# Optimization experiments

Measured on AMD Instinct MI355X. Metric: run time of the kernel, lower is better.

Reference implementation:

```python
import jax, jax.numpy as jnp
import numpy as np

B, S, D, H, DK, F, L, V = 4, 128, 512, 8, 64, 2048, 2, 32000
N = B * S  # nodes per side (enc and dec each)


def _pe():
    pos = np.arange(S, dtype=np.float32)[:, None]
    div = np.exp(-np.log(10000.0) * np.arange(0, D, 2, dtype=np.float32) / D)
    pe = np.zeros((S, D), dtype=np.float32)
    pe[:, 0::2] = np.sin(pos * div)
    pe[:, 1::2] = np.cos(pos * div)
    return jnp.asarray(np.tile(pe, (B, 1)))  # [N, D]


def _ln(x, g, b, eps=1e-5):
    mu = jnp.mean(x, -1, keepdims=True)
    var = jnp.mean(jnp.square(x - mu), -1, keepdims=True)
    return g * (x - mu) * jax.lax.rsqrt(var + eps) + b


def _edge_attn(q, k, v, src, dst, n_dst):
    # src_dot_dst('k','q','score') then scaled_exp, then src_mul_edge + sum scatter
    s = jnp.sum(k[src] * q[dst], -1, keepdims=True) / np.float32(np.sqrt(DK))  # [E,H,1]
    s = jnp.exp(jnp.clip(s, -10.0, 10.0))
    wv = jax.ops.segment_sum(v[src] * s, dst, num_segments=n_dst)  # [n_dst,H,DK]
    z = jax.ops.segment_sum(s, dst, num_segments=n_dst)            # [n_dst,H,1]
    return wv / z


def _attn_block(x_q, x_kv, Wq, Wk, Wv, Wo, src, dst):
    q = (x_q @ Wq).reshape(-1, H, DK)
    k = (x_kv @ Wk).reshape(-1, H, DK)
    v = (x_kv @ Wv).reshape(-1, H, DK)
    o = _edge_attn(q, k, v, src, dst, x_q.shape[0]).reshape(-1, D)
    return o @ Wo


def _forward(p, src_tok, tgt_tok, ee_src, ee_dst, dd_src, dd_dst, ed_src, ed_dst):
    (src_emb, tgt_emb, enc_Wqkv, enc_Wo, enc_ln1, enc_W1, enc_b1, enc_W2, enc_b2,
     enc_ln2, enc_lnf, dec_Wqkv, dec_Wo, dec_ln1, dec_cWq, dec_cWkv, dec_cWo,
     dec_ln2, dec_W1, dec_b1, dec_W2, dec_b2, dec_ln3, dec_lnf, gen_W, gen_b) = p
    pe = _pe()
    scale = np.float32(np.sqrt(D))
    x_e = src_emb[src_tok].reshape(N, D) * scale + pe  # token + positional embed
    x_d = tgt_emb[tgt_tok].reshape(N, D) * scale + pe
    for l in range(L):  # encoder layers (ee edges)
        xn = _ln(x_e, enc_ln1[l, 0], enc_ln1[l, 1])
        x_e = x_e + _attn_block(xn, xn, enc_Wqkv[l, 0], enc_Wqkv[l, 1], enc_Wqkv[l, 2], enc_Wo[l], ee_src, ee_dst)
        xn = _ln(x_e, enc_ln2[l, 0], enc_ln2[l, 1])
        x_e = x_e + jax.nn.relu(xn @ enc_W1[l] + enc_b1[l]) @ enc_W2[l] + enc_b2[l]
    x_e = _ln(x_e, enc_lnf[0], enc_lnf[1])
    for l in range(L):  # decoder layers: self (dd) then cross (ed)
        xn = _ln(x_d, dec_ln1[l, 0], dec_ln1[l, 1])
        x_d = x_d + _attn_block(xn, xn, dec_Wqkv[l, 0], dec_Wqkv[l, 1], dec_Wqkv[l, 2], dec_Wo[l], dd_src, dd_dst)
        xn = _ln(x_d, dec_ln2[l, 0], dec_ln2[l, 1])
        x_d = x_d + _attn_block(xn, x_e, dec_cWq[l], dec_cWkv[l, 0], dec_cWkv[l, 1], dec_cWo[l], ed_src, ed_dst)
        xn = _ln(x_d, dec_ln3[l, 0], dec_ln3[l, 1])
        x_d = x_d + jax.nn.relu(xn @ dec_W1[l] + dec_b1[l]) @ dec_W2[l] + dec_b2[l]
    x_d = _ln(x_d, dec_lnf[0], dec_lnf[1])
    return jax.nn.log_softmax(x_d @ gen_W + gen_b, axis=-1)  # generator


def setup_inputs():
    key = jax.random.key(0)
    ks = iter(jax.random.split(key, 32))
    w = lambda *shape: jax.random.normal(next(ks), shape, jnp.float32) * 0.02
    lnp = lambda n: jnp.tile(jnp.stack([jnp.ones(D), jnp.zeros(D)])[None], (n, 1, 1))
    # structured edge lists: per-sentence blocks
    i, j = np.meshgrid(np.arange(S), np.arange(S), indexing='ij')  # src pos, dst pos
    base = (np.arange(B)[:, None] * S).astype(np.int32)
    full_s = (base + i.ravel()[None, :]).ravel().astype(np.int32)
    full_d = (base + j.ravel()[None, :]).ravel().astype(np.int32)
    m = i.ravel() <= j.ravel()  # causal mask for dec self-attention
    dd_s = (base + i.ravel()[m][None, :]).ravel().astype(np.int32)
    dd_d = (base + j.ravel()[m][None, :]).ravel().astype(np.int32)
    k1, k2 = jax.random.split(next(ks))
    return dict(
        src_emb=w(V, D), tgt_emb=w(V, D),
        enc_Wqkv=w(L, 3, D, D), enc_Wo=w(L, D, D), enc_ln1=lnp(L),
        enc_W1=w(L, D, F), enc_b1=jnp.zeros((L, F)), enc_W2=w(L, F, D),
        enc_b2=jnp.zeros((L, D)), enc_ln2=lnp(L), enc_lnf=lnp(1)[0],
        dec_Wqkv=w(L, 3, D, D), dec_Wo=w(L, D, D), dec_ln1=lnp(L),
        dec_cWq=w(L, D, D), dec_cWkv=w(L, 2, D, D), dec_cWo=w(L, D, D), dec_ln2=lnp(L),
        dec_W1=w(L, D, F), dec_b1=jnp.zeros((L, F)), dec_W2=w(L, F, D),
        dec_b2=jnp.zeros((L, D)), dec_ln3=lnp(L), dec_lnf=lnp(1)[0],
        gen_W=w(D, V), gen_b=jnp.zeros((V,)),
        src_tok=jax.random.randint(k1, (B, S), 0, V, jnp.int32),
        tgt_tok=jax.random.randint(k2, (B, S), 0, V, jnp.int32),
        ee_src=jnp.asarray(full_s), ee_dst=jnp.asarray(full_d),
        dd_src=jnp.asarray(dd_s), dd_dst=jnp.asarray(dd_d),
        ed_src=jnp.asarray(full_s), ed_dst=jnp.asarray(full_d),
    )


def reference(src_emb, tgt_emb, enc_Wqkv, enc_Wo, enc_ln1, enc_W1, enc_b1, enc_W2,
              enc_b2, enc_ln2, enc_lnf, dec_Wqkv, dec_Wo, dec_ln1, dec_cWq,
              dec_cWkv, dec_cWo, dec_ln2, dec_W1, dec_b1, dec_W2, dec_b2,
              dec_ln3, dec_lnf, gen_W, gen_b, src_tok, tgt_tok, ee_src, ee_dst,
              dd_src, dd_dst, ed_src, ed_dst):
    p = (src_emb, tgt_emb, enc_Wqkv, enc_Wo, enc_ln1, enc_W1, enc_b1, enc_W2,
         enc_b2, enc_ln2, enc_lnf, dec_Wqkv, dec_Wo, dec_ln1, dec_cWq, dec_cWkv,
         dec_cWo, dec_ln2, dec_W1, dec_b1, dec_W2, dec_b2, dec_ln3, dec_lnf,
         gen_W, gen_b)
    return _forward(p, src_tok, tgt_tok, ee_src, ee_dst, dd_src, dd_dst, ed_src, ed_dst)
```

## Files before the change

kernel.cpp:

```cpp
#include <hip/hip_runtime.h>
#include <cstddef>

constexpr int cB = 4, cS = 128, cD = 512, cH = 8, cDK = 64, cF = 2048, cL = 2, cV = 32000;
constexpr int cN = cB * cS;

typedef __attribute__((ext_vector_type(8)))  short short8;
typedef __attribute__((ext_vector_type(4)))  float f32x4;
typedef __attribute__((ext_vector_type(16))) float f32x16;

__device__ __forceinline__ short f2bf(float x) {
    unsigned u = __builtin_bit_cast(unsigned, x);
    unsigned r = (u + 0x7fffu + ((u >> 16) & 1u)) >> 16;
    return (short)r;
}
__device__ __forceinline__ short f2h(float x) {
    return __builtin_bit_cast(short, (_Float16)x);
}
__device__ __forceinline__ float h2f(short s) {
    return (float)__builtin_bit_cast(_Float16, s);
}

__device__ __forceinline__ void bar_lgkm() {
    asm volatile("s_waitcnt lgkmcnt(0)" ::: "memory");
    __builtin_amdgcn_s_barrier();
    asm volatile("" ::: "memory");
}

__global__ __launch_bounds__(256) void embed_k(const float* __restrict__ e0,
                                               const int* __restrict__ t0,
                                               float* __restrict__ X0,
                                               const float* __restrict__ e1,
                                               const int* __restrict__ t1,
                                               float* __restrict__ X1)
{
    const float* emb = blockIdx.z ? e1 : e0;
    const int* tok   = blockIdx.z ? t1 : t0;
    float* X         = blockIdx.z ? X1 : X0;
    int n = blockIdx.x;
    int tid = threadIdx.x;
    int t = tok[n];
    int pos = n & (cS - 1);
    const float scale = 22.62741699796952f;
    for (int d = tid; d < cD; d += 256) {
        int i2 = d & ~1;
        float div = expf(-9.210340371976184f * (float)i2 / (float)cD);
        float arg = (float)pos * div;
        float p = (d & 1) ? cosf(arg) : sinf(arg);
        X[(long)n * cD + d] = emb[(long)t * cD + d] * scale + p;
    }
}

__global__ __launch_bounds__(256) void ln_k(const float* __restrict__ X,
                                            const float* __restrict__ g,
                                            const float* __restrict__ bta,
                                            short* __restrict__ Yb)
{
    __shared__ float red[256];
    int row = blockIdx.x, tid = threadIdx.x;
    const float* x = X + (long)row * cD;
    float v0 = x[tid], v1 = x[tid + 256];

    red[tid] = v0 + v1;
    __syncthreads();
    for (int st = 128; st > 0; st >>= 1) { if (tid < st) red[tid] += red[tid + st]; __syncthreads(); }
    float mu = red[0] * (1.0f / (float)cD);
    __syncthreads();

    float d0 = v0 - mu, d1 = v1 - mu;
    red[tid] = d0 * d0 + d1 * d1;
    __syncthreads();
    for (int st = 128; st > 0; st >>= 1) { if (tid < st) red[tid] += red[tid + st]; __syncthreads(); }
    float var = red[0] * (1.0f / (float)cD);
    float rs = rsqrtf(var + 1e-5f);

    Yb[(long)row * cD + tid]       = f2bf(g[tid]       * d0 * rs + bta[tid]);
    Yb[(long)row * cD + tid + 256] = f2bf(g[tid + 256] * d1 * rs + bta[tid + 256]);
}

struct TCP { const float* s[24]; };

__global__ __launch_bounds__(256) void tconv_k(TCP ptrs, short* __restrict__ dst,
                                               int K, int N)
{
    __shared__ float t[64][65];
    const float* s = ptrs.s[blockIdx.z];
    short* d = dst + (long)blockIdx.z * K * N;
    int k0 = blockIdx.y * 64, n0 = blockIdx.x * 64;
    int tid = threadIdx.x;
    const f32x4* s4 = (const f32x4*)s;
#pragma unroll
    for (int i = 0; i < 4; i++) {
        int lin = tid + i * 256;
        int r = lin >> 4, c4 = lin & 15;
        f32x4 v = s4[(long)(k0 + r) * (N >> 2) + (n0 >> 2) + c4];
        t[r][c4 * 4 + 0] = v[0]; t[r][c4 * 4 + 1] = v[1];
        t[r][c4 * 4 + 2] = v[2]; t[r][c4 * 4 + 3] = v[3];
    }
    __syncthreads();
#pragma unroll
    for (int i = 0; i < 2; i++) {
        int lin = tid + i * 256;
        int r = lin >> 3, c8 = lin & 7;
        short8 o;
#pragma unroll
        for (int j = 0; j < 8; j++) o[j] = f2bf(t[c8 * 8 + j][r]);
        *(short8*)&d[(long)(n0 + r) * K + k0 + c8 * 8] = o;
    }
}

template <int MR, int NR, bool LNF, int KSTEPS>
__global__ __launch_bounds__(512) void gemm8_k(
    const short* __restrict__ Abf, const float* __restrict__ Af,
    const float* __restrict__ lng, const float* __restrict__ lnb,
    const float* __restrict__ Af2, const float* __restrict__ lng2,
    const float* __restrict__ lnb2, int zsplit,
    const short* __restrict__ Bt,
    const float* __restrict__ bias, const float* __restrict__ res,
    float* __restrict__ C, short* __restrict__ Cb,
    int N, int relu, long aStride, long btStride, long cStride)
{
    constexpr int K = KSTEPS * 128;
    constexpr int BM = MR * 32, BN = NR * 32, PITCH = 136;
    constexpr int ACH = (BM * 128) / (8 * 512);
    constexpr int BCH = (BN * 128) / (8 * 512);
    static_assert(ACH >= 1 && BCH >= 1, "tile too small");
    static_assert(!LNF || KSTEPS <= 4, "LNF only on short-K path");
    __shared__ short As[2][BM * PITCH];
    __shared__ short Bs[2][BN * PITCH];
    __shared__ float red[4][64][MR * NR * 4];
    __shared__ float mu_s[BM], rs_s[BM];
    __shared__ float gb_s[2][LNF ? 512 : 8];

    const int z = blockIdx.z;
    const float* Afz = (LNF && z >= zsplit) ? Af2 : Af;
    const float* gz  = (LNF && z >= zsplit) ? lng2 : lng;
    const float* bz  = (LNF && z >= zsplit) ? lnb2 : lnb;
    const short* Am = Abf ? (Abf + (long)z * aStride) : nullptr;
    const short* Bm = Bt + (long)z * btStride;
    int tid = threadIdx.x;
    int lane = tid & 63, wid = tid >> 6;
    int grp = wid >> 2, quad = wid & 3;
    int wr = quad >> 1, wc = quad & 1;
    int m0 = blockIdx.y * BM, n0 = blockIdx.x * BN;
    int lrow = lane & 15, koff = (lane >> 4) * 8;
    const int Kh = K >> 1;

    f32x4 acc[MR][NR];
#pragma unroll
    for (int m = 0; m < MR; m++)
#pragma unroll
        for (int n = 0; n < NR; n++) acc[m][n] = f32x4{0.f, 0.f, 0.f, 0.f};

    constexpr int FAN = LNF ? ACH * 2 : 1;

    auto stageA = [&](int step, short8 (&qa)[ACH], f32x4 (&fa)[FAN]) {
#pragma unroll
        for (int i = 0; i < ACH; i++) {
            int lin = tid + i * 512, r = lin >> 4, c8 = lin & 15;
            int kg = (c8 < 8) ? (step * 64 + c8 * 8) : (Kh + step * 64 + (c8 - 8) * 8);
            if constexpr (LNF) {
                const f32x4* p = (const f32x4*)(Afz + (long)(m0 + r) * K + kg);
                fa[2 * i] = p[0]; fa[2 * i + 1] = p[1];
            } else {
                qa[i] = *(const short8*)&Am[(long)(m0 + r) * K + kg];
            }
        }
    };
    auto stageB = [&](int step, short8 (&qb)[BCH]) {
#pragma unroll
        for (int i = 0; i < BCH; i++) {
            int lin = tid + i * 512, r = lin >> 4, c8 = lin & 15;
            int kg = (c8 < 8) ? (step * 64 + c8 * 8) : (Kh + step * 64 + (c8 - 8) * 8);
            qb[i] = *(const short8*)&Bm[(long)(n0 + r) * K + kg];
        }
    };
    auto writeT = [&](int buf, int step, short8 (&qa)[ACH], f32x4 (&fa)[FAN],
                      short8 (&qb)[BCH]) {
#pragma unroll
        for (int i = 0; i < ACH; i++) {
            int lin = tid + i * 512, r = lin >> 4, c8 = lin & 15;
            if constexpr (LNF) {
                int kg = (c8 < 8) ? (step * 64 + c8 * 8) : (Kh + step * 64 + (c8 - 8) * 8);
                float mu = mu_s[r], rs = rs_s[r];
                short8 o;
#pragma unroll
                for (int j = 0; j < 4; j++)
                    o[j] = f2bf((fa[2 * i][j] - mu) * rs * gb_s[0][kg + j] + gb_s[1][kg + j]);
#pragma unroll
                for (int j = 0; j < 4; j++)
                    o[4 + j] = f2bf((fa[2 * i + 1][j] - mu) * rs * gb_s[0][kg + 4 + j] + gb_s[1][kg + 4 + j]);
                *(short8*)&As[buf][r * PITCH + c8 * 8] = o;
            } else {
                *(short8*)&As[buf][r * PITCH + c8 * 8] = qa[i];
            }
        }
#pragma unroll
        for (int i = 0; i < BCH; i++) {
            int lin = tid + i * 512, r = lin >> 4, c8 = lin & 15;
            *(short8*)&Bs[buf][r * PITCH + c8 * 8] = qb[i];
        }
    };
    auto mfmaStep = [&](int buf) {
#pragma unroll
        for (int kk2 = 0; kk2 < 2; kk2++) {
            int kk = grp * 64 + kk2 * 32;
            short8 a[MR], b[NR];
#pragma unroll
            for (int m = 0; m < MR; m++)
                a[m] = *(const short8*)&As[buf][(wr * MR * 16 + m * 16 + lrow) * PITCH + kk + koff];
#pragma unroll
            for (int n = 0; n < NR; n++)
                b[n] = *(const short8*)&Bs[buf][(wc * NR * 16 + n * 16 + lrow) * PITCH + kk + koff];
#pragma unroll
            for (int m = 0; m < MR; m++)
#pragma unroll
                for (int n = 0; n < NR; n++)
                    acc[m][n] = __builtin_amdgcn_mfma_f32_16x16x32_bf16(a[m], b[n], acc[m][n], 0, 0, 0);
        }
    };
    auto lnProlog = [&]() {
        if constexpr (LNF) {
            constexpr int TPR = 512 / BM;
            int r = tid / TPR, sub = tid % TPR;
            const f32x4* row4 = (const f32x4*)(Afz + (long)(m0 + r) * K);
            float s = 0.f, s2 = 0.f;
            for (int i = sub; i < (K >> 2); i += TPR) {
                f32x4 v = row4[i];
                s  += v[0] + v[1] + v[2] + v[3];
                s2 += v[0] * v[0] + v[1] * v[1] + v[2] * v[2] + v[3] * v[3];
            }
#pragma unroll
            for (int o = TPR >> 1; o > 0; o >>= 1) {
                s += __shfl_xor(s, o); s2 += __shfl_xor(s2, o);
            }
            if (sub == 0) {
                float mu = s / (float)K;
                float var = s2 / (float)K - mu * mu;
                mu_s[r] = mu; rs_s[r] = rsqrtf(var + 1e-5f);
            }
            if (tid < 512) { gb_s[0][tid] = gz[tid]; gb_s[1][tid] = bz[tid]; }
            bar_lgkm();
        }
    };

    if constexpr (KSTEPS <= 4) {
        short8 qa[KSTEPS][ACH], qb[KSTEPS][BCH];
        f32x4 fa[LNF ? KSTEPS : 1][FAN];
#pragma unroll
        for (int s = 0; s < KSTEPS; s++) {
            stageA(s, qa[s], fa[LNF ? s : 0]);
            stageB(s, qb[s]);
        }
        lnProlog();
#pragma unroll
        for (int s = 0; s < KSTEPS; s++) {
            writeT(s & 1, s, qa[s], fa[LNF ? s : 0], qb[s]);
            bar_lgkm();
            mfmaStep(s & 1);
            if (s + 1 < KSTEPS) bar_lgkm();
        }
    } else {
        short8 qa0[ACH], qa1[ACH], qb0[BCH], qb1[BCH];
        f32x4 fdum[FAN];
        stageA(0, qa0, fdum); stageB(0, qb0);
        stageA(1, qa1, fdum); stageB(1, qb1);
        int st = 0;
        for (;;) {
            writeT(0, st, qa0, fdum, qb0);
            if (st + 2 < KSTEPS) { stageA(st + 2, qa0, fdum); stageB(st + 2, qb0); }
            bar_lgkm();
            mfmaStep(0);
            st++; if (st >= KSTEPS) break;

            writeT(1, st, qa1, fdum, qb1);
            if (st + 2 < KSTEPS) { stageA(st + 2, qa1, fdum); stageB(st + 2, qb1); }
            bar_lgkm();
            mfmaStep(1);
            st++; if (st >= KSTEPS) break;
        }
    }

    __syncthreads();
    if (grp == 1) {
#pragma unroll
        for (int m = 0; m < MR; m++)
#pragma unroll
            for (int n = 0; n < NR; n++)
#pragma unroll
                for (int j = 0; j < 4; j++)
                    red[quad][lane][(m * NR + n) * 4 + j] = acc[m][n][j];
    }
    __syncthreads();
    if (grp == 0) {
#pragma unroll
        for (int m = 0; m < MR; m++) {
            int rbase = m0 + wr * MR * 16 + m * 16 + (lane >> 4) * 4;
#pragma unroll
            for (int n = 0; n < NR; n++) {
                int col = n0 + wc * NR * 16 + n * 16 + (lane & 15);
                float bv = bias ? bias[col] : 0.f;
#pragma unroll
                for (int j = 0; j < 4; j++) {
                    long row = rbase + j;
                    long off = row * N + col + (long)z * cStride;
                    float v = acc[m][n][j] + red[quad][lane][(m * NR + n) * 4 + j] + bv;
                    if (res)  v += res[off];
                    if (relu) v = fmaxf(v, 0.f);
                    if (C)  C[off] = v;
                    if (Cb) Cb[off] = f2bf(v);
                }
            }
        }
    }
}

__global__ __launch_bounds__(256) void attn_k(const short* __restrict__ Qb,
                                              const short* __restrict__ Kb,
                                              const short* __restrict__ Vb,
                                              short* __restrict__ Ob,
                                              int causMask, long sQKV, long sO)
{
    __shared__ short q_s[64 * 72];
    __shared__ short k_s[128 * 72];
    __shared__ short vt_s[64 * 128];
    __shared__ short p_s[64 * 136];
    __shared__ float z_s[64];

    int tid = threadIdx.x, lane = tid & 63, wid = tid >> 6;
    int lr = lane & 15, lg = lane >> 4;
    int h = blockIdx.x, b = blockIdx.y;
    int stream = blockIdx.z >> 1, dstBase = (blockIdx.z & 1) * 64;
    int causal = (causMask >> stream) & 1;
    const short* Q = Qb + (long)stream * sQKV;
    const short* Km = Kb + (long)stream * sQKV;
    const short* Vm = Vb + (long)stream * sQKV;
    short* O = Ob + (long)stream * sO;
    const int RS = cH * cDK;
    long qbase = ((long)b * cS + dstBase) * RS + h * cDK;
    long kbase = ((long)b * cS) * RS + h * cDK;

#pragma unroll
    for (int i = 0; i < 2; i++) {
        int lin = tid + i * 256, t = lin >> 3, c8 = lin & 7;
        *(short8*)&q_s[t * 72 + c8 * 8] = *(const short8*)&Q[qbase + (long)t * RS + c8 * 8];
    }
#pragma unroll
    for (int i = 0; i < 4; i++) {
        int lin = tid + i * 256, t = lin >> 3, c8 = lin & 7;
        *(short8*)&k_s[t * 72 + c8 * 8] = *(const short8*)&Km[kbase + (long)t * RS + c8 * 8];
    }
#pragma unroll
    for (int i = 0; i < 4; i++) {
        int lin = tid + i * 256, src = lin >> 3, c8 = lin & 7;
        short8 v = *(const short8*)&Vm[kbase + (long)src * RS + c8 * 8];
#pragma unroll
        for (int j = 0; j < 8; j++) {
            int dk = c8 * 8 + j;
            int g = (src >> 3) ^ (dk >> 3);
            vt_s[dk * 128 + g * 8 + (src & 7)] = v[j];
        }
    }
    bar_lgkm();

    f32x4 sacc[8];
#pragma unroll
    for (int n = 0; n < 8; n++) sacc[n] = f32x4{0.f, 0.f, 0.f, 0.f};
#pragma unroll
    for (int kk = 0; kk < 64; kk += 32) {
        short8 a = *(const short8*)&q_s[(wid * 16 + lr) * 72 + kk + lg * 8];
#pragma unroll
        for (int n = 0; n < 8; n++) {
            short8 bf = *(const short8*)&k_s[(n * 16 + lr) * 72 + kk + lg * 8];
            sacc[n] = __builtin_amdgcn_mfma_f32_16x16x32_bf16(a, bf, sacc[n], 0, 0, 0);
        }
    }
    float z[4] = {0.f, 0.f, 0.f, 0.f};
#pragma unroll
    for (int n = 0; n < 8; n++) {
        int src = n * 16 + lr;
#pragma unroll
        for (int j = 0; j < 4; j++) {
            int dst = dstBase + wid * 16 + lg * 4 + j;
            float s = sacc[n][j] * 0.125f;
            s = __expf(fminf(fmaxf(s, -10.f), 10.f));
            if (causal && src > dst) s = 0.f;
            sacc[n][j] = s;
            z[j] += s;
        }
    }
#pragma unroll
    for (int j = 0; j < 4; j++) {
        z[j] += __shfl_xor(z[j], 1); z[j] += __shfl_xor(z[j], 2);
        z[j] += __shfl_xor(z[j], 4); z[j] += __shfl_xor(z[j], 8);
    }
#pragma unroll
    for (int n = 0; n < 8; n++) {
        int src = n * 16 + lr;
#pragma unroll
        for (int j = 0; j < 4; j++)
            p_s[(wid * 16 + lg * 4 + j) * 136 + src] = f2bf(sacc[n][j]);
    }
    if (lr == 0) {
#pragma unroll
        for (int j = 0; j < 4; j++) z_s[wid * 16 + lg * 4 + j] = z[j];
    }
    bar_lgkm();

    f32x4 oacc[4];
#pragma unroll
    for (int n = 0; n < 4; n++) oacc[n] = f32x4{0.f, 0.f, 0.f, 0.f};
#pragma unroll
    for (int kk = 0; kk < 128; kk += 32) {
        int dkr = wid * 16 + lr;
        int g = ((kk >> 3) + lg) ^ (dkr >> 3);
        short8 a = *(const short8*)&vt_s[dkr * 128 + g * 8];
#pragma unroll
        for (int n = 0; n < 4; n++) {
            short8 bf = *(const short8*)&p_s[(n * 16 + lr) * 136 + kk + lg * 8];
            oacc[n] = __builtin_amdgcn_mfma_f32_16x16x32_bf16(a, bf, oacc[n], 0, 0, 0);
        }
    }
#pragma unroll
    for (int n = 0; n < 4; n++) {
        int dl = n * 16 + lr;
        float zz = z_s[dl];
#pragma unroll
        for (int j = 0; j < 4; j++) {
            int dk = wid * 16 + lg * 4 + j;
            O[qbase + (long)dl * RS + dk] = f2bf(oacc[n][j] / zz);
        }
    }
}

__global__ __launch_bounds__(256) void gen32_k(
    const short* __restrict__ A, const short* __restrict__ Bt,
    const float* __restrict__ bias, short* __restrict__ Ch, int N, int K)
{
    constexpr int PITCH = 72;
    constexpr int ACH = 4, BCH = 4;
    __shared__ short As[2][128 * PITCH];
    __shared__ short Bs[2][128 * PITCH];

    int bx = blockIdx.x, by = blockIdx.y;
    {
        int nb = gridDim.x * gridDim.y;
        int bid = by * gridDim.x + bx;
        int w = (bid & 7) * (nb >> 3) + (bid >> 3);
        by = w % gridDim.y; bx = w / gridDim.y;
    }
    int tid = threadIdx.x;
    int lane = tid & 63, wid = tid >> 6;
    int wr = wid >> 1, wc = wid & 1;
    int m0 = by * 128, n0 = bx * 128;
    int l31 = lane & 31, l5 = lane >> 5;

    f32x16 acc[2][2];
#pragma unroll
    for (int m = 0; m < 2; m++)
#pragma unroll
        for (int n = 0; n < 2; n++)
#pragma unroll
            for (int r = 0; r < 16; r++) acc[m][n][r] = 0.f;

    short8 qa0[ACH], qa1[ACH], qb0[BCH], qb1[BCH];
    auto stage = [&](int k0, short8 (&qa)[ACH], short8 (&qb)[BCH]) {
#pragma unroll
        for (int i = 0; i < ACH; i++) {
            int lin = tid + i * 256, r = lin >> 3, c8 = lin & 7;
            qa[i] = *(const short8*)&A[(long)(m0 + r) * K + k0 + c8 * 8];
        }
#pragma unroll
        for (int i = 0; i < BCH; i++) {
            int lin = tid + i * 256, r = lin >> 3, c8 = lin & 7;
            qb[i] = *(const short8*)&Bt[(long)(n0 + r) * K + k0 + c8 * 8];
        }
    };
    auto writeT = [&](int buf, short8 (&qa)[ACH], short8 (&qb)[BCH]) {
#pragma unroll
        for (int i = 0; i < ACH; i++) {
            int lin = tid + i * 256, r = lin >> 3, c8 = lin & 7;
            *(short8*)&As[buf][r * PITCH + c8 * 8] = qa[i];
        }
#pragma unroll
        for (int i = 0; i < BCH; i++) {
            int lin = tid + i * 256, r = lin >> 3, c8 = lin & 7;
            *(short8*)&Bs[buf][r * PITCH + c8 * 8] = qb[i];
        }
    };
    auto mfmaStep = [&](int buf) {
#pragma unroll
        for (int kk = 0; kk < 64; kk += 16) {
            short8 a[2], b[2];
#pragma unroll
            for (int m = 0; m < 2; m++)
                a[m] = *(const short8*)&As[buf][(wr * 64 + m * 32 + l31) * PITCH + kk + l5 * 8];
#pragma unroll
            for (int n = 0; n < 2; n++)
                b[n] = *(const short8*)&Bs[buf][(wc * 64 + n * 32 + l31) * PITCH + kk + l5 * 8];
#pragma unroll
            for (int m = 0; m < 2; m++)
#pragma unroll
                for (int n = 0; n < 2; n++)
                    acc[m][n] = __builtin_amdgcn_mfma_f32_32x32x16_bf16(a[m], b[n], acc[m][n], 0, 0, 0);
        }
    };

    const int steps = K >> 6;
    stage(0, qa0, qb0);
    stage(64, qa1, qb1);
    int st = 0;
    for (;;) {
        writeT(0, qa0, qb0);
        if (st + 2 < steps) stage((st + 2) * 64, qa0, qb0);
        bar_lgkm();
        mfmaStep(0);
        st++; if (st >= steps) break;

        writeT(1, qa1, qb1);
        if (st + 2 < steps) stage((st + 2) * 64, qa1, qb1);
        bar_lgkm();
        mfmaStep(1);
        st++; if (st >= steps) break;
    }

#pragma unroll
    for (int m = 0; m < 2; m++) {
#pragma unroll
        for (int n = 0; n < 2; n++) {
            int col = n0 + wc * 64 + n * 32 + l31;
            float bv = bias[col];
#pragma unroll
            for (int r = 0; r < 16; r++) {
                int row = m0 + wr * 64 + m * 32 + (r & 3) + 8 * (r >> 2) + 4 * l5;
                Ch[(long)row * N + col] = f2h(acc[m][n][r] + bv);
            }
        }
    }
}

__global__ __launch_bounds__(256) void lsm_k(const short* __restrict__ L16,
                                             float* __restrict__ Out)
{
    __shared__ float rm[256], rs[256];
    int row = blockIdx.x, tid = threadIdx.x;
    const short8* x8 = (const short8*)(L16 + (long)row * cV);
    float* o = Out + (long)row * cV;
    constexpr int NV = cV / 8;

    float m = -1e30f, s = 0.f;
    for (int i = tid; i < NV; i += 256) {
        short8 v = x8[i];
        float f[8];
#pragma unroll
        for (int j = 0; j < 8; j++) f[j] = h2f(v[j]);
        float cm = f[0];
#pragma unroll
        for (int j = 1; j < 8; j++) cm = fmaxf(cm, f[j]);
        float nm = fmaxf(m, cm);
        float a = 0.f;
#pragma unroll
        for (int j = 0; j < 8; j++) a += __expf(f[j] - nm);
        s = s * __expf(m - nm) + a;
        m = nm;
    }
    rm[tid] = m; rs[tid] = s;
    __syncthreads();
    for (int st = 128; st > 0; st >>= 1) {
        if (tid < st) {
            float m2 = rm[tid + st], s2 = rs[tid + st];
            float nm = fmaxf(rm[tid], m2);
            rs[tid] = rs[tid] * __expf(rm[tid] - nm) + s2 * __expf(m2 - nm);
            rm[tid] = nm;
        }
        __syncthreads();
    }
    float lse = rm[0] + __logf(rs[0]);

    for (int i = tid; i < NV; i += 256) {
        short8 v = x8[i];
        f32x4 o0, o1;
#pragma unroll
        for (int j = 0; j < 4; j++) o0[j] = h2f(v[j]) - lse;
#pragma unroll
        for (int j = 0; j < 4; j++) o1[j] = h2f(v[4 + j]) - lse;
        *(f32x4*)&o[i * 8]     = o0;
        *(f32x4*)&o[i * 8 + 4] = o1;
    }
}

extern "C" void kernel_launch(void* const* d_in, const int* in_sizes, int n_in,
                              void* d_out, int out_size, void* d_ws, size_t ws_size,
                              hipStream_t stream)
{
    const float* src_emb  = (const float*)d_in[0];
    const float* tgt_emb  = (const float*)d_in[1];
    const float* enc_Wqkv = (const float*)d_in[2];
    const float* enc_Wo   = (const float*)d_in[3];
    const float* enc_ln1  = (const float*)d_in[4];
    const float* enc_W1   = (const float*)d_in[5];
    const float* enc_b1   = (const float*)d_in[6];
    const float* enc_W2   = (const float*)d_in[7];
    const float* enc_b2   = (const float*)d_in[8];
    const float* enc_ln2  = (const float*)d_in[9];
    const float* enc_lnf  = (const float*)d_in[10];
    const float* dec_Wqkv = (const float*)d_in[11];
    const float* dec_Wo   = (const float*)d_in[12];
    const float* dec_ln1  = (const float*)d_in[13];
    const float* dec_cWq  = (const float*)d_in[14];
    const float* dec_cWkv = (const float*)d_in[15];
    const float* dec_cWo  = (const float*)d_in[16];
    const float* dec_ln2  = (const float*)d_in[17];
    const float* dec_W1   = (const float*)d_in[18];
    const float* dec_b1   = (const float*)d_in[19];
    const float* dec_W2   = (const float*)d_in[20];
    const float* dec_b2   = (const float*)d_in[21];
    const float* dec_ln3  = (const float*)d_in[22];
    const float* dec_lnf  = (const float*)d_in[23];
    const float* gen_W    = (const float*)d_in[24];
    const float* gen_b    = (const float*)d_in[25];
    const int* src_tok    = (const int*)d_in[26];
    const int* tgt_tok    = (const int*)d_in[27];

    const long ND = (long)cN * cD;
    const long DD = (long)cD * cD;
    const long DF = (long)cD * cF;

    float* x_e = (float*)d_ws;
    float* x_d = x_e + ND;

    short* qkv6  = (short*)(x_d + ND);
    short* ob2   = qkv6 + 6 * ND;
    short* hb_bf = ob2 + 2 * ND;
    short* kvc   = hb_bf + (long)cN * cF;
    short* xn_bf = kvc + 4 * ND;
    short* wDD  = xn_bf + ND;
    short* wDF  = wDD + 24 * DD;
    short* wFD  = wDF + 4 * DF;
    short* genT = wFD + 4 * DF;
    short* lg16 = genT + (long)cD * cV;

    {
        TCP p{};
        int i = 0;
        for (int j = 0; j < 3; j++) p.s[i++] = enc_Wqkv + (long)j * DD;
        for (int j = 0; j < 3; j++) p.s[i++] = dec_Wqkv + (long)j * DD;
        p.s[i++] = enc_Wo; p.s[i++] = dec_Wo;
        for (int j = 3; j < 6; j++) p.s[i++] = enc_Wqkv + (long)j * DD;
        p.s[i++] = dec_cWq;
        for (int j = 3; j < 6; j++) p.s[i++] = dec_Wqkv + (long)j * DD;
        p.s[i++] = enc_Wo + DD;
        p.s[i++] = dec_Wo + DD;
        p.s[i++] = dec_cWq + DD;
        for (int j = 0; j < 4; j++) p.s[i++] = dec_cWkv + (long)j * DD;
        for (int j = 0; j < 2; j++) p.s[i++] = dec_cWo  + (long)j * DD;
        tconv_k<<<dim3(cD / 64, cD / 64, 24), 256, 0, stream>>>(p, wDD, cD, cD);
    }
    {
        TCP p{};
        p.s[0] = enc_W1; p.s[1] = enc_W1 + DF; p.s[2] = dec_W1; p.s[3] = dec_W1 + DF;
        tconv_k<<<dim3(cF / 64, cD / 64, 4), 256, 0, stream>>>(p, wDF, cD, cF);
    }
    {
        TCP p{};
        p.s[0] = enc_W2; p.s[1] = enc_W2 + DF; p.s[2] = dec_W2; p.s[3] = dec_W2 + DF;
        tconv_k<<<dim3(cD / 64, cF / 64, 4), 256, 0, stream>>>(p, wFD, cF, cD);
    }
    {
        TCP p{};
        p.s[0] = gen_W;
        tconv_k<<<dim3(cV / 64, cD / 64, 1), 256, 0, stream>>>(p, genT, cD, cV);
    }

    embed_k<<<dim3(cN, 1, 2), 256, 0, stream>>>(src_emb, src_tok, x_e,
                                                tgt_emb, tgt_tok, x_d);

    dim3 gDD(cD / 32, cN / 32);
    dim3 gFFN1(cF / 64, cN / 64);

    gemm8_k<1, 1, true, 4><<<dim3(cD / 32, cN / 32, 6), 512, 0, stream>>>(
        nullptr, x_e, enc_ln1, enc_ln1 + cD,
        x_d, dec_ln1, dec_ln1 + cD, 3,
        wDD, nullptr, nullptr, nullptr, qkv6, cD, 0, 0, DD, ND);
    attn_k<<<dim3(cH, cB, 4), 256, 0, stream>>>(
        qkv6, qkv6 + ND, qkv6 + 2 * ND, ob2, 0b10, 3 * ND, ND);
    gemm8_k<1, 1, false, 4><<<dim3(cD / 32, cN / 32, 2), 512, 0, stream>>>(
        ob2, nullptr, nullptr, nullptr, nullptr, nullptr, nullptr, 99,
        wDD + 6 * DD, nullptr, x_e, x_e, nullptr, cD, 0, ND, DD, ND);

    gemm8_k<2, 2, true, 4><<<gFFN1, 512, 0, stream>>>(
        nullptr, x_e, enc_ln2, enc_ln2 + cD, nullptr, nullptr, nullptr, 99,
        wDF, enc_b1, nullptr, nullptr, hb_bf, cF, 1, 0, 0, 0);
    gemm8_k<1, 1, false, 16><<<gDD, 512, 0, stream>>>(
        hb_bf, nullptr, nullptr, nullptr, nullptr, nullptr, nullptr, 99,
        wFD, enc_b2, x_e, x_e, nullptr, cD, 0, 0, 0, 0);

    gemm8_k<1, 1, true, 4><<<dim3(cD / 32, cN / 32, 4), 512, 0, stream>>>(
        nullptr, x_e, enc_ln1 + 2 * cD, enc_ln1 + 3 * cD,
        x_d, dec_ln2, dec_ln2 + cD, 3,
        wDD + 8 * DD, nullptr, nullptr, nullptr, qkv6, cD, 0, 0, DD, ND);
    attn_k<<<dim3(cH, cB, 2), 256, 0, stream>>>(
        qkv6, qkv6 + ND, qkv6 + 2 * ND, ob2, 0, 0, 0);
    gemm8_k<1, 1, false, 4><<<gDD, 512, 0, stream>>>(
        ob2, nullptr, nullptr, nullptr, nullptr, nullptr, nullptr, 99,
        wDD + 15 * DD, nullptr, x_e, x_e, nullptr, cD, 0, 0, 0, 0);
    gemm8_k<2, 2, true, 4><<<gFFN1, 512, 0, stream>>>(
        nullptr, x_e, enc_ln2 + 2 * cD, enc_ln2 + 3 * cD,
        nullptr, nullptr, nullptr, 99,
        wDF + DF, enc_b1 + cF, nullptr, nullptr, hb_bf, cF, 1, 0, 0, 0);
    gemm8_k<1, 1, false, 16><<<gDD, 512, 0, stream>>>(
        hb_bf, nullptr, nullptr, nullptr, nullptr, nullptr, nullptr, 99,
        wFD + DF, enc_b2 + cD, x_e, x_e, nullptr, cD, 0, 0, 0, 0);

    gemm8_k<1, 1, true, 4><<<dim3(cD / 32, cN / 32, 4), 512, 0, stream>>>(
        nullptr, x_e, enc_lnf, enc_lnf + cD, nullptr, nullptr, nullptr, 99,
        wDD + 18 * DD, nullptr, nullptr, nullptr, kvc, cD, 0, 0, DD, ND);

    attn_k<<<dim3(cH, cB, 2), 256, 0, stream>>>(
        qkv6 + 3 * ND, kvc, kvc + ND, ob2, 0, 0, 0);
    gemm8_k<1, 1, false, 4><<<gDD, 512, 0, stream>>>(
        ob2, nullptr, nullptr, nullptr, nullptr, nullptr, nullptr, 99,
        wDD + 22 * DD, nullptr, x_d, x_d, nullptr, cD, 0, 0, 0, 0);
    gemm8_k<2, 2, true, 4><<<gFFN1, 512, 0, stream>>>(
        nullptr, x_d, dec_ln3, dec_ln3 + cD, nullptr, nullptr, nullptr, 99,
        wDF + 2 * DF, dec_b1, nullptr, nullptr, hb_bf, cF, 1, 0, 0, 0);
    gemm8_k<1, 1, false, 16><<<gDD, 512, 0, stream>>>(
        hb_bf, nullptr, nullptr, nullptr, nullptr, nullptr, nullptr, 99,
        wFD + 2 * DF, dec_b2, x_d, x_d, nullptr, cD, 0, 0, 0, 0);

    gemm8_k<1, 1, true, 4><<<dim3(cD / 32, cN / 32, 3), 512, 0, stream>>>(
        nullptr, x_d, dec_ln1 + 2 * cD, dec_ln1 + 3 * cD,
        nullptr, nullptr, nullptr, 99,
        wDD + 12 * DD, nullptr, nullptr, nullptr, qkv6, cD, 0, 0, DD, ND);
    attn_k<<<dim3(cH, cB, 2), 256, 0, stream>>>(
        qkv6, qkv6 + ND, qkv6 + 2 * ND, ob2, 1, 0, 0);
    gemm8_k<1, 1, false, 4><<<gDD, 512, 0, stream>>>(
        ob2, nullptr, nullptr, nullptr, nullptr, nullptr, nullptr, 99,
        wDD + 16 * DD, nullptr, x_d, x_d, nullptr, cD, 0, 0, 0, 0);
    gemm8_k<1, 1, true, 4><<<gDD, 512, 0, stream>>>(
        nullptr, x_d, dec_ln2 + 2 * cD, dec_ln2 + 3 * cD,
        nullptr, nullptr, nullptr, 99,
        wDD + 17 * DD, nullptr, nullptr, nullptr, qkv6, cD, 0, 0, 0, 0);
    attn_k<<<dim3(cH, cB, 2), 256, 0, stream>>>(
        qkv6, kvc + 2 * ND, kvc + 3 * ND, ob2, 0, 0, 0);
    gemm8_k<1, 1, false, 4><<<gDD, 512, 0, stream>>>(
        ob2, nullptr, nullptr, nullptr, nullptr, nullptr, nullptr, 99,
        wDD + 23 * DD, nullptr, x_d, x_d, nullptr, cD, 0, 0, 0, 0);
    gemm8_k<2, 2, true, 4><<<gFFN1, 512, 0, stream>>>(
        nullptr, x_d, dec_ln3 + 2 * cD, dec_ln3 + 3 * cD,
        nullptr, nullptr, nullptr, 99,
        wDF + 3 * DF, dec_b1 + cF, nullptr, nullptr, hb_bf, cF, 1, 0, 0, 0);
    gemm8_k<1, 1, false, 16><<<gDD, 512, 0, stream>>>(
        hb_bf, nullptr, nullptr, nullptr, nullptr, nullptr, nullptr, 99,
        wFD + 3 * DF, dec_b2 + cD, x_d, x_d, nullptr, cD, 0, 0, 0, 0);

    ln_k<<<cN, 256, 0, stream>>>(x_d, dec_lnf, dec_lnf + cD, xn_bf);
    gen32_k<<<dim3(cV / 128, cN / 128), 256, 0, stream>>>(
        xn_bf, genT, gen_b, lg16, cV, cD);
    lsm_k<<<cN, 256, 0, stream>>>(lg16, (float*)d_out);
}
```

Before: 308.7 us.

## Load generator GEMM fragments directly from global memory, bypassing LDS

The vocab-projection GEMM no longer stages A and B tiles through shared memory with barriers. Each wave now loads its MFMA operand fragments straight from global memory into registers, double-buffered across 64-wide K steps, with the K loop fully unrolled and hardcoded to 512. This removes LDS writes, LDS reads and block barriers. In exchange there is no cross-wave reuse, so each operand row is fetched by two waves (more global/L2 traffic), the per-lane loads are 16-byte strided, and the kernel now assumes K equals 512.

```diff
diff --git a/kernel.cpp b/kernel.cpp
--- a/kernel.cpp
+++ b/kernel.cpp
@@ -436,11 +436,6 @@
     const short* __restrict__ A, const short* __restrict__ Bt,
     const float* __restrict__ bias, short* __restrict__ Ch, int N, int K)
 {
-    constexpr int PITCH = 72;
-    constexpr int ACH = 4, BCH = 4;
-    __shared__ short As[2][128 * PITCH];
-    __shared__ short Bs[2][128 * PITCH];
-
     int bx = blockIdx.x, by = blockIdx.y;
     {
         int nb = gridDim.x * gridDim.y;
@@ -454,6 +449,12 @@
     int m0 = by * 128, n0 = bx * 128;
     int l31 = lane & 31, l5 = lane >> 5;
 
+    const short* Ar0 = A  + (long)(m0 + wr * 64 + l31) * K;
+    const short* Ar1 = Ar0 + (long)32 * K;
+    const short* Br0 = Bt + (long)(n0 + wc * 64 + l31) * K;
+    const short* Br1 = Br0 + (long)32 * K;
+    int ko = l5 * 8;
+
     f32x16 acc[2][2];
 #pragma unroll
     for (int m = 0; m < 2; m++)
@@ -462,65 +463,35 @@
 #pragma unroll
             for (int r = 0; r < 16; r++) acc[m][n][r] = 0.f;
 
-    short8 qa0[ACH], qa1[ACH], qb0[BCH], qb1[BCH];
-    auto stage = [&](int k0, short8 (&qa)[ACH], short8 (&qb)[BCH]) {
-#pragma unroll
-        for (int i = 0; i < ACH; i++) {
-            int lin = tid + i * 256, r = lin >> 3, c8 = lin & 7;
-            qa[i] = *(const short8*)&A[(long)(m0 + r) * K + k0 + c8 * 8];
-        }
-#pragma unroll
-        for (int i = 0; i < BCH; i++) {
-            int lin = tid + i * 256, r = lin >> 3, c8 = lin & 7;
-            qb[i] = *(const short8*)&Bt[(long)(n0 + r) * K + k0 + c8 * 8];
+    short8 a0[2][4], b0[2][4], a1[2][4], b1[2][4];
+    auto load = [&](int k0, short8 (&fa)[2][4], short8 (&fb)[2][4]) {
+#pragma unroll
+        for (int q = 0; q < 4; q++) {
+            fa[0][q] = *(const short8*)&Ar0[k0 + q * 16 + ko];
+            fa[1][q] = *(const short8*)&Ar1[k0 + q * 16 + ko];
+            fb[0][q] = *(const short8*)&Br0[k0 + q * 16 + ko];
+            fb[1][q] = *(const short8*)&Br1[k0 + q * 16 + ko];
         }
     };
-    auto writeT = [&](int buf, short8 (&qa)[ACH], short8 (&qb)[BCH]) {
-#pragma unroll
-        for (int i = 0; i < ACH; i++) {
-            int lin = tid + i * 256, r = lin >> 3, c8 = lin & 7;
-            *(short8*)&As[buf][r * PITCH + c8 * 8] = qa[i];
-        }
-#pragma unroll
-        for (int i = 0; i < BCH; i++) {
-            int lin = tid + i * 256, r = lin >> 3, c8 = lin & 7;
-            *(short8*)&Bs[buf][r * PITCH + c8 * 8] = qb[i];
-        }
+    auto step = [&](short8 (&fa)[2][4], short8 (&fb)[2][4]) {
+#pragma unroll
+        for (int q = 0; q < 4; q++)
+#pragma unroll
+            for (int m = 0; m < 2; m++)
+#pragma unroll
+                for (int n = 0; n < 2; n++)
+                    acc[m][n] = __builtin_amdgcn_mfma_f32_32x32x16_bf16(
+                        fa[m][q], fb[n][q], acc[m][n], 0, 0, 0);
     };
-    auto mfmaStep = [&](int buf) {
-#pragma unroll
-        for (int kk = 0; kk < 64; kk += 16) {
-            short8 a[2], b[2];
-#pragma unroll
-            for (int m = 0; m < 2; m++)
-                a[m] = *(const short8*)&As[buf][(wr * 64 + m * 32 + l31) * PITCH + kk + l5 * 8];
-#pragma unroll
-            for (int n = 0; n < 2; n++)
-                b[n] = *(const short8*)&Bs[buf][(wc * 64 + n * 32 + l31) * PITCH + kk + l5 * 8];
-#pragma unroll
-            for (int m = 0; m < 2; m++)
-#pragma unroll
-                for (int n = 0; n < 2; n++)
-                    acc[m][n] = __builtin_amdgcn_mfma_f32_32x32x16_bf16(a[m], b[n], acc[m][n], 0, 0, 0);
-        }
-    };
-
-    const int steps = K >> 6;
-    stage(0, qa0, qb0);
-    stage(64, qa1, qb1);
-    int st = 0;
-    for (;;) {
-        writeT(0, qa0, qb0);
-        if (st + 2 < steps) stage((st + 2) * 64, qa0, qb0);
-        bar_lgkm();
-        mfmaStep(0);
-        st++; if (st >= steps) break;
-
-        writeT(1, qa1, qb1);
-        if (st + 2 < steps) stage((st + 2) * 64, qa1, qb1);
-        bar_lgkm();
-        mfmaStep(1);
-        st++; if (st >= steps) break;
+
+    load(0, a0, b0);
+    load(64, a1, b1);
+#pragma unroll
+    for (int k0 = 0; k0 < 512; k0 += 128) {
+        step(a0, b0);
+        if (k0 + 128 < 512) load(k0 + 128, a0, b0);
+        step(a1, b1);
+        if (k0 + 192 < 512) load(k0 + 192, a1, b1);
     }
 
 #pragma unroll
```

Result: slower. 336.5 us (+9.0%).
